# Kernel optimization log

Hardware: AMD Instinct MI355X
Metric: run time of the kernel (lower is better)

The kernel has to match this reference:

```python
import jax, jax.numpy as jnp
import numpy as np
import math

D_MODEL = 512
N_HEADS = 8
D_FF = 2048
TOP_FACTOR = 5
LN_EPS = 1e-5


def _layernorm(x, g, b):
    m = jnp.mean(x, axis=-1, keepdims=True)
    v = jnp.mean((x - m) ** 2, axis=-1, keepdims=True)
    return (x - m) / jnp.sqrt(v + LN_EPS) * g + b


def _prob_sparse_attn(q_in, k_in, v_in, wq, bq, wk, bk, wv, bv, wo, bo):
    # weights stored (in, out): y = x @ w + b  (equivalent to torch Linear)
    B, Lq, dm = q_in.shape
    Lk = k_in.shape[1]
    H, D = N_HEADS, dm // N_HEADS
    q = (q_in @ wq + bq).reshape(B, Lq, H, D).transpose(0, 2, 1, 3)  # (B,H,Lq,D)
    k = (k_in @ wk + bk).reshape(B, Lk, H, D).transpose(0, 2, 1, 3)
    v = (v_in @ wv + bv).reshape(B, Lk, H, D).transpose(0, 2, 1, 3)

    qn = q / jnp.linalg.norm(q, axis=-1, keepdims=True)
    kn = k / jnp.linalg.norm(k, axis=-1, keepdims=True)
    # full cosine-similarity matrix, reduced to a row mean (as in the original)
    scores_all = jnp.einsum('bhqd,bhkd->bhqk', qn, kn)
    mean_scores = scores_all.mean(axis=-1)  # (B,H,Lq)

    u = max(1, Lq // TOP_FACTOR)
    _, top_idx = jax.lax.top_k(mean_scores, u)  # (B,H,u)

    q_sel = jnp.take_along_axis(q, top_idx[..., None], axis=2)  # (B,H,u,D)
    scores = jnp.einsum('bhud,bhkd->bhuk', q_sel, k) / math.sqrt(D)
    attn = jax.nn.softmax(scores, axis=-1)
    ctx_sel = jnp.einsum('bhuk,bhkd->bhud', attn, v)  # (B,H,u,D)

    b_ix = jnp.arange(B)[:, None, None]
    h_ix = jnp.arange(H)[None, :, None]
    context = jnp.zeros((B, H, Lq, D), dtype=q.dtype).at[b_ix, h_ix, top_idx].set(ctx_sel)
    out = context.transpose(0, 2, 1, 3).reshape(B, Lq, dm)
    return out @ wo + bo


def _decoder_layer(x, enc_out, p):
    xn = _layernorm(x, p['ln1_g'], p['ln1_b'])
    x = x + _prob_sparse_attn(xn, xn, xn, p['sa_wq'], p['sa_bq'], p['sa_wk'], p['sa_bk'],
                              p['sa_wv'], p['sa_bv'], p['sa_wo'], p['sa_bo'])
    xn = _layernorm(x, p['ln2_g'], p['ln2_b'])
    x = x + _prob_sparse_attn(xn, enc_out, enc_out, p['ca_wq'], p['ca_bq'], p['ca_wk'], p['ca_bk'],
                              p['ca_wv'], p['ca_bv'], p['ca_wo'], p['ca_bo'])
    xn = _layernorm(x, p['ln3_g'], p['ln3_b'])
    h = jax.nn.relu(xn @ p['ff_w1'] + p['ff_b1'])
    return x + (h @ p['ff_w2'] + p['ff_b2'])


def setup_inputs() -> dict:
    key = jax.random.key(0)
    ks = iter(jax.random.split(key, 32))
    B, L = 2, 2048
    dm, dff = D_MODEL, D_FF
    s = 1.0 / math.sqrt(dm)
    inp = {
        'x': jax.random.normal(next(ks), (B, L, dm), jnp.float32),
        'enc_out': jax.random.normal(next(ks), (B, L, dm), jnp.float32),
    }
    for pre in ('sa', 'ca'):
        for nm in ('wq', 'wk', 'wv', 'wo'):
            inp[f'{pre}_{nm}'] = jax.random.normal(next(ks), (dm, dm), jnp.float32) * s
            inp[f'{pre}_{nm[1:] and "b" + nm[1:]}'] = jnp.zeros((dm,), jnp.float32)
    inp['ff_w1'] = jax.random.normal(next(ks), (dm, dff), jnp.float32) * s
    inp['ff_b1'] = jnp.zeros((dff,), jnp.float32)
    inp['ff_w2'] = jax.random.normal(next(ks), (dff, dm), jnp.float32) / math.sqrt(dff)
    inp['ff_b2'] = jnp.zeros((dm,), jnp.float32)
    for i in (1, 2, 3):
        inp[f'ln{i}_g'] = jnp.ones((dm,), jnp.float32)
        inp[f'ln{i}_b'] = jnp.zeros((dm,), jnp.float32)
    return inp


def reference(x, enc_out,
              sa_wq, sa_bq, sa_wk, sa_bk, sa_wv, sa_bv, sa_wo, sa_bo,
              ca_wq, ca_bq, ca_wk, ca_bk, ca_wv, ca_bv, ca_wo, ca_bo,
              ff_w1, ff_b1, ff_w2, ff_b2,
              ln1_g, ln1_b, ln2_g, ln2_b, ln3_g, ln3_b):
    p = dict(sa_wq=sa_wq, sa_bq=sa_bq, sa_wk=sa_wk, sa_bk=sa_bk, sa_wv=sa_wv, sa_bv=sa_bv,
             sa_wo=sa_wo, sa_bo=sa_bo, ca_wq=ca_wq, ca_bq=ca_bq, ca_wk=ca_wk, ca_bk=ca_bk,
             ca_wv=ca_wv, ca_bv=ca_bv, ca_wo=ca_wo, ca_bo=ca_bo,
             ff_w1=ff_w1, ff_b1=ff_b1, ff_w2=ff_w2, ff_b2=ff_b2,
             ln1_g=ln1_g, ln1_b=ln1_b, ln2_g=ln2_g, ln2_b=ln2_b, ln3_g=ln3_g, ln3_b=ln3_b)
    return _decoder_layer(x, enc_out, p)
```

## Files before the change

### kernel.cpp

```cpp
#include <hip/hip_runtime.h>

#define BB 2
#define LL 2048
#define DM 512
#define NH 8
#define DH 64
#define DFF 2048
#define UU 409
#define ROWS (BB*LL)
#define X_ELEMS 2097152
#define NCHUNK 16

typedef unsigned short u16;
typedef __attribute__((ext_vector_type(8))) short short8;
typedef __attribute__((ext_vector_type(4))) float floatx4;

#define G_TOTAL 38200000
__device__ float g_buf[G_TOTAL];
__device__ int   g_isbf16;

#define A_Q     10495488
#define A_K     12592640
#define A_V     14689792
#define A_MKN   25175552
#define A_MS    25176576
#define A_RANK  25209344
#define A_PARTK 25242112
#define A_LIST  25274880
#define A_PO    25281536
#define A_PML   33670144
#define A_CTXF  16786944
#define XN_H    16796672
#define XN_L    18893824
#define CTX_H   33573888
#define CTX_L   35671040
#define ENC_H   37768192
#define ENC_L   39865344
#define AH_H    41962496
#define WT_SAQKV 67864576
#define WT_SAO   69437440
#define WT_CAQ   69961728
#define WT_CAKV  70486016
#define WT_CAO   71534592
#define WT_W1    72058880
#define WT_W2    74156032

__constant__ int c_end[28] = {
    2097152, 4194304, 4456448, 4456960, 4719104, 4719616, 4981760, 4982272,
    5244416, 5244928, 5507072, 5507584, 5769728, 5770240, 6032384, 6032896,
    6295040, 6295552, 7344128, 7346176, 8394752, 8395264, 8395776, 8396288,
    8396800, 8397312, 8397824, 8398336
};
__constant__ int sm_idx[16] = {3,5,7,9,11,13,15,17,19,21,22,23,24,25,26,27};
__constant__ int sm_cum[16] = {64,128,192,256,320,384,448,512,768,832,896,960,1024,1088,1152,1216};
#define XG 262144
#define EG 262144
#define SG 1216

__device__ __forceinline__ float bf2f(u16 x) {
    union { unsigned int u; float f; } c; c.u = ((unsigned int)x) << 16; return c.f;
}
__device__ __forceinline__ u16 f2bf(float f) {
    union { float f; unsigned int u; } c; c.f = f;
    unsigned int u = c.u;
    return (u16)((u + 0x7FFFu + ((u >> 16) & 1u)) >> 16);
}

struct P28 { const void* p[28]; };
struct I3 { int v[3]; };

__constant__ int tj[10][6] = {
    {2,  WT_SAQKV, 0,    512,  786432, 8},
    {4,  WT_SAQKV, 512,  512,  786432, 8},
    {6,  WT_SAQKV, 1024, 512,  786432, 8},
    {8,  WT_SAO,   0,    512,  262144, 8},
    {10, WT_CAQ,   0,    512,  262144, 8},
    {12, WT_CAKV,  0,    512,  524288, 8},
    {14, WT_CAKV,  512,  512,  524288, 8},
    {16, WT_CAO,   0,    512,  262144, 8},
    {18, WT_W1,    0,    512, 1048576, 32},
    {20, WT_W2,    0,   2048, 1048576, 8},
};
__constant__ int tcum[10] = {64, 128, 192, 256, 320, 384, 448, 512, 768, 1024};
__global__ void prep_all(P28 ps) {
    const int f = (((const u16*)ps.p[22])[0] == 0x3F80u) ? 1 : 0;
    if (blockIdx.x == 0 && threadIdx.x == 0) g_isbf16 = f;
    u16* gb16 = (u16*)g_buf;
    if (blockIdx.x < 1024) {
        int bid = blockIdx.x;
        int j = 0;
        while (bid >= tcum[j]) j++;
        int t = bid - (j ? tcum[j - 1] : 0);
        int widx = tj[j][0], wt = tj[j][1], col0 = tj[j][2];
        int K = tj[j][3], lo = tj[j][4], txn = tj[j][5];
        int Nsrc = txn * 64;
        int n0 = (t % txn) * 64, k0 = (t / txn) * 64;
        __shared__ float tb[64][65];
        int c = threadIdx.x & 63, r0 = threadIdx.x >> 6;
        const void* W = ps.p[widx];
        u16* WTh = gb16 + wt;
        for (int i = 0; i < 16; i++) {
            int r = r0 + 4 * i;
            size_t src = (size_t)(k0 + r) * Nsrc + n0 + c;
            tb[r][c] = f ? bf2f(((const u16*)W)[src]) : ((const float*)W)[src];
        }
        __syncthreads();
        for (int i = 0; i < 16; i++) {
            int r = r0 + 4 * i;
            float v = tb[c][r];
            u16 hi = f2bf(v);
            size_t o = (size_t)(col0 + n0 + r) * K + k0 + c;
            WTh[o] = hi;
            WTh[lo + o] = f2bf(v - bf2f(hi));
        }
        return;
    }
    int stride = 2048 * blockDim.x;
    for (int g = (blockIdx.x - 1024) * blockDim.x + threadIdx.x; g < XG + EG + SG; g += stride) {
        if (g < XG) {
            int e = g * 8;
            if (f) {
                uint4 raw = ((const uint4*)ps.p[0])[g];
                const u16* rr = (const u16*)&raw;
                float v[8] __attribute__((aligned(16)));
#pragma unroll
                for (int i = 0; i < 8; i++) v[i] = bf2f(rr[i]);
                *(float4*)(g_buf + e) = ((const float4*)v)[0];
                *(float4*)(g_buf + e + 4) = ((const float4*)v)[1];
            } else {
                *(uint4*)(g_buf + e)     = ((const uint4*)ps.p[0])[g * 2];
                *(uint4*)(g_buf + e + 4) = ((const uint4*)ps.p[0])[g * 2 + 1];
            }
        } else if (g < XG + EG) {
            int gl = g - XG;
            int e = gl * 8;
            float v[8] __attribute__((aligned(16)));
            if (f) {
                uint4 raw = ((const uint4*)ps.p[1])[gl];
                const u16* rr = (const u16*)&raw;
#pragma unroll
                for (int i = 0; i < 8; i++) v[i] = bf2f(rr[i]);
            } else {
                *(float4*)(v)     = ((const float4*)ps.p[1])[gl * 2];
                *(float4*)(v + 4) = ((const float4*)ps.p[1])[gl * 2 + 1];
            }
            u16 hh[8] __attribute__((aligned(16)));
            u16 lo[8] __attribute__((aligned(16)));
#pragma unroll
            for (int i = 0; i < 8; i++) { u16 hi = f2bf(v[i]); hh[i] = hi; lo[i] = f2bf(v[i] - bf2f(hi)); }
            *(uint4*)(&gb16[ENC_H + e]) = *(const uint4*)hh;
            *(uint4*)(&gb16[ENC_L + e]) = *(const uint4*)lo;
        } else {
            int t = g - XG - EG;
            int si = 0;
            while (t >= sm_cum[si]) si++;
            int s = sm_idx[si];
            int gl = t - (si ? sm_cum[si - 1] : 0);
            int e = gl * 8;
            float* dst = g_buf + c_end[s - 1] + e;
            if (f) {
                uint4 raw = *(const uint4*)((const u16*)ps.p[s] + e);
                const u16* rr = (const u16*)&raw;
#pragma unroll
                for (int i = 0; i < 8; i++) dst[i] = bf2f(rr[i]);
            } else {
                *(uint4*)(dst)     = *(const uint4*)((const float*)ps.p[s] + e);
                *(uint4*)(dst + 4) = *(const uint4*)((const float*)ps.p[s] + e + 4);
            }
        }
    }
}

__global__ void lnorm_k(int x_off, int g_off, int b_off, int yh_u16, int yl_u16) {
    int row = blockIdx.x;
    int tid = threadIdx.x;
    const float* x = g_buf + x_off + (size_t)row * DM;
    float a = x[tid], c = x[tid + 256];
    float s1 = a + c, s2 = a * a + c * c;
    for (int o = 32; o > 0; o >>= 1) { s1 += __shfl_xor(s1, o); s2 += __shfl_xor(s2, o); }
    __shared__ float r1[4], r2[4];
    int wave = tid >> 6, lane = tid & 63;
    if (lane == 0) { r1[wave] = s1; r2[wave] = s2; }
    __syncthreads();
    s1 = r1[0] + r1[1] + r1[2] + r1[3];
    s2 = r2[0] + r2[1] + r2[2] + r2[3];
    float mean = s1 * (1.0f / DM);
    float var  = s2 * (1.0f / DM) - mean * mean;
    float rstd = rsqrtf(var + 1e-5f);
    const float* gg = g_buf + g_off;
    const float* bb = g_buf + b_off;
    u16* yh = ((u16*)g_buf) + yh_u16 + (size_t)row * DM;
    u16* yl = ((u16*)g_buf) + yl_u16 + (size_t)row * DM;
    float v1 = (a - mean) * rstd * gg[tid]       + bb[tid];
    float v2 = (c - mean) * rstd * gg[tid + 256] + bb[tid + 256];
    u16 h1 = f2bf(v1), h2 = f2bf(v2);
    yh[tid] = h1;       yl[tid] = f2bf(v1 - bf2f(h1));
    yh[tid + 256] = h2; yl[tid + 256] = f2bf(v2 - bf2f(h2));
}

template<int WM, bool SPLIT, bool SEC, bool RELU, bool RESID, bool FINAL, bool OUTH>
__global__ void mgemm_k(I3 a_offs, I3 splt, I3 alz, int wt_u16_off, I3 boffs, int resid_off,
                        int out_off, void* __restrict__ dext, int M, int N, int K) {
    constexpr int BT_M = WM * 32;
    constexpr int A4 = BT_M * 4;
    __shared__ u16 Ash[BT_M * 40];
    __shared__ u16 Asl[SPLIT ? BT_M * 40 : 8];
    __shared__ u16 Bsh[128 * 40];
    __shared__ u16 Bsl[SPLIT ? 128 * 40 : 8];
    int sec_blk = SEC ? ((blockIdx.x * 128) >> 9) : 0;
    const u16* Ah = ((const u16*)g_buf) + a_offs.v[sec_blk];
    const u16* Al = Ah + (size_t)M * K;
    const u16* WTh = ((const u16*)g_buf) + wt_u16_off;
    const u16* WTl = WTh + (size_t)N * K;
    const int isbf = g_isbf16;
    const bool use_al = SPLIT && splt.v[sec_blk] && !(alz.v[sec_blk] && isbf);
    const bool use_bl = SPLIT && splt.v[sec_blk] && !isbf;
    int tid = threadIdx.x;
    int lane = tid & 63, wid = tid >> 6;
    int wm = wid >> 1, wn = wid & 1;
    int quad = lane >> 4, l15 = lane & 15;
    int m0 = blockIdx.y * BT_M, n0 = blockIdx.x * 128;
    floatx4 acc[WM][4];
#pragma unroll
    for (int i = 0; i < WM; i++)
#pragma unroll
        for (int j = 0; j < 4; j++) acc[i][j] = (floatx4){0.f, 0.f, 0.f, 0.f};
    for (int k0 = 0; k0 < K; k0 += 32) {
#pragma unroll
        for (int i = 0; i < (A4 + 255) / 256; i++) {
            int idx8 = tid + 256 * i;
            if (A4 % 256 == 0 || idx8 < A4) {
                int r = idx8 >> 2, c8 = (idx8 & 3) * 8;
                *(uint4*)(&Ash[r * 40 + c8]) = *(const uint4*)(Ah + (size_t)(m0 + r) * K + k0 + c8);
                if (SPLIT && use_al)
                    *(uint4*)(&Asl[r * 40 + c8]) = *(const uint4*)(Al + (size_t)(m0 + r) * K + k0 + c8);
            }
        }
#pragma unroll
        for (int i = 0; i < 2; i++) {
            int idx8 = tid + 256 * i;
            int r = idx8 >> 2, c8 = (idx8 & 3) * 8;
            *(uint4*)(&Bsh[r * 40 + c8]) = *(const uint4*)(WTh + (size_t)(n0 + r) * K + k0 + c8);
            if (SPLIT && use_bl)
                *(uint4*)(&Bsl[r * 40 + c8]) = *(const uint4*)(WTl + (size_t)(n0 + r) * K + k0 + c8);
        }
        __syncthreads();
        short8 ah[WM], bh[4], al[WM], bl[4];
#pragma unroll
        for (int i = 0; i < WM; i++) {
            int ro = (wm * WM * 16 + i * 16 + l15) * 40 + quad * 8;
            ah[i] = *(const short8*)(&Ash[ro]);
            if (SPLIT && use_al) al[i] = *(const short8*)(&Asl[ro]);
        }
#pragma unroll
        for (int j = 0; j < 4; j++) {
            int ro = (wn * 64 + j * 16 + l15) * 40 + quad * 8;
            bh[j] = *(const short8*)(&Bsh[ro]);
            if (SPLIT && use_bl) bl[j] = *(const short8*)(&Bsl[ro]);
        }
#pragma unroll
        for (int i = 0; i < WM; i++)
#pragma unroll
            for (int j = 0; j < 4; j++) {
                acc[i][j] = __builtin_amdgcn_mfma_f32_16x16x32_bf16(ah[i], bh[j], acc[i][j], 0, 0, 0);
                if constexpr (SPLIT) {
                    if (use_bl)
                        acc[i][j] = __builtin_amdgcn_mfma_f32_16x16x32_bf16(ah[i], bl[j], acc[i][j], 0, 0, 0);
                    if (use_al)
                        acc[i][j] = __builtin_amdgcn_mfma_f32_16x16x32_bf16(al[i], bh[j], acc[i][j], 0, 0, 0);
                }
            }
        __syncthreads();
    }
#pragma unroll
    for (int i = 0; i < WM; i++)
#pragma unroll
        for (int j = 0; j < 4; j++)
#pragma unroll
            for (int r = 0; r < 4; r++) {
                int row = m0 + wm * WM * 16 + i * 16 + quad * 4 + r;
                int col = n0 + wn * 64 + j * 16 + l15;
                int sec = SEC ? (col >> 9) : 0;
                int ci  = SEC ? (col & 511) : col;
                float v = acc[i][j][r] + g_buf[boffs.v[sec] + ci];
                if (RELU) v = fmaxf(v, 0.f);
                if (RESID) v += g_buf[resid_off + (size_t)row * N + col];
                if (FINAL) {
                    if (g_isbf16) ((u16*)dext)[(size_t)row * N + col] = f2bf(v);
                    else          ((float*)dext)[(size_t)row * N + col] = v;
                } else if (OUTH) {
                    ((u16*)g_buf)[out_off + (size_t)row * N + col] = f2bf(v);
                } else if (SEC) {
                    g_buf[out_off + ((size_t)sec * ROWS + row) * 512 + ci] = v;
                } else {
                    g_buf[out_off + (size_t)row * N + col] = v;
                }
            }
}

__global__ void meankn_p1(int k_off, int part_off) {
    int bh = blockIdx.x >> 5, chunk = blockIdx.x & 31;
    int b = bh >> 3, h = bh & 7;
    int wave = threadIdx.x >> 6, lane = threadIdx.x & 63;
    const float* base = g_buf + k_off + (size_t)b * LL * DM + (size_t)h * DH + lane;
    float acc = 0.f;
    for (int t = 0; t < 16; t++) {
        int j = chunk * 64 + wave * 16 + t;
        float kv = base[(size_t)j * DM];
        float s = kv * kv;
        for (int o = 32; o > 0; o >>= 1) s += __shfl_xor(s, o);
        acc += kv / sqrtf(fmaxf(s, 1e-30f));
    }
    __shared__ float red[4][64];
    red[wave][lane] = acc;
    __syncthreads();
    if (threadIdx.x < 64)
        g_buf[part_off + (size_t)blockIdx.x * 64 + threadIdx.x] =
            red[0][threadIdx.x] + red[1][threadIdx.x] + red[2][threadIdx.x] + red[3][threadIdx.x];
}

__global__ void mscore_k(int q_off, int part_off, int ms_off) {
    int bh = blockIdx.y, b = bh >> 3, h = bh & 7;
    int tid = threadIdx.x;
    __shared__ float mk[64];
    if (tid < 64) {
        float s = 0.f;
        for (int c = 0; c < 32; c++) s += g_buf[part_off + (size_t)(bh * 32 + c) * 64 + tid];
        mk[tid] = s * (1.0f / LL);
    }
    __syncthreads();
    int w = tid >> 6, lane = tid & 63;
    float m = mk[lane];
#pragma unroll
    for (int it = 0; it < 8; it++) {
        int row = blockIdx.x * 32 + it * 4 + w;
        float qv = g_buf[q_off + ((size_t)b * LL + row) * DM + h * DH + lane];
        float s = qv * qv, d = qv * m;
        for (int o = 32; o > 0; o >>= 1) { s += __shfl_xor(s, o); d += __shfl_xor(d, o); }
        if (lane == 0) g_buf[ms_off + bh * LL + row] = d / sqrtf(fmaxf(s, 1e-30f));
    }
}

__global__ void topsel_k(int ms_off, int list_off, int rank_off, int u) {
    __shared__ float s[LL];
    int bh = blockIdx.y, chunk = blockIdx.x;
    for (int i = threadIdx.x; i < LL; i += 256) s[i] = g_buf[ms_off + bh * LL + i];
    __syncthreads();
    int il = threadIdx.x >> 2;
    int i = chunk * 64 + il;
    int jq = threadIdx.x & 3;
    float si = s[i];
    int cnt = 0;
    for (int t = 0; t < 512; t++) {
        int j = jq * 512 + t;
        float sj = s[j];
        cnt += (sj > si) || (sj == si && j < i);
    }
    cnt += __shfl_xor(cnt, 1);
    cnt += __shfl_xor(cnt, 2);
    if (jq == 0) {
        int* list = (int*)(g_buf + list_off);
        int* rank = (int*)(g_buf + rank_off);
        if (cnt < u) { list[bh * 416 + cnt] = i; rank[bh * LL + i] = cnt; }
        else rank[bh * LL + i] = -1;
    }
}

template<bool S3>
__global__ __launch_bounds__(256) void attn_flash(int q_off, int k_off, int v_off,
        int list_off, int po_off, int pml_off, int u) {
    int bh = blockIdx.y, b = bh >> 3, h = bh & 7;
    int chunk = blockIdx.z;
    int tid = threadIdx.x, lane = tid & 63, w = tid >> 6;
    int quad = lane >> 4, l15 = lane & 15;
    const int* list = (const int*)(g_buf + list_off);

    short8 qh[2][2], ql[2][2];
#pragma unroll
    for (int g = 0; g < 2; g++) {
        int slot_q = blockIdx.x * 128 + w * 32 + g * 16 + l15;
        int qidx = list[bh * 416 + (slot_q < u ? slot_q : u - 1)];
        const float* qp = g_buf + q_off + ((size_t)b * LL + qidx) * DM + h * DH;
#pragma unroll
        for (int d2 = 0; d2 < 2; d2++) {
            float v[8] __attribute__((aligned(16)));
            *(float4*)(v)     = *(const float4*)(qp + d2 * 32 + quad * 8);
            *(float4*)(v + 4) = *(const float4*)(qp + d2 * 32 + quad * 8 + 4);
            u16 hh[8] __attribute__((aligned(16)));
            u16 lo[8] __attribute__((aligned(16)));
#pragma unroll
            for (int j = 0; j < 8; j++) {
                float s = v[j] * 0.125f;
                u16 hi = f2bf(s); hh[j] = hi; lo[j] = f2bf(s - bf2f(hi));
            }
            qh[g][d2] = *(const short8*)hh; ql[g][d2] = *(const short8*)lo;
        }
    }

    __shared__ u16 Ksh[64 * 68];
    __shared__ u16 Ksl[S3 ? 64 * 68 : 8];
    __shared__ u16 Vth[64 * 68];
    __shared__ u16 Vtl[S3 ? 64 * 68 : 8];
    __shared__ float smbuf[4352];

    float m_run[2][4], l_run[2][4];
    floatx4 acc_o[2][4];
#pragma unroll
    for (int g = 0; g < 2; g++)
#pragma unroll
        for (int r = 0; r < 4; r++) {
            m_run[g][r] = -3.0e38f; l_run[g][r] = 0.f;
            acc_o[g][r] = (floatx4){0.f, 0.f, 0.f, 0.f};
        }

    for (int kt = 0; kt < 2; kt++) {
        int row0 = chunk * 128 + kt * 64;
        __syncthreads();
        {
            int tok = tid >> 2, c = (tid & 3) * 16;
            const float* kp = g_buf + k_off + ((size_t)(b * LL + row0 + tok)) * DM + h * DH + c;
            float v[16] __attribute__((aligned(16)));
#pragma unroll
            for (int i = 0; i < 4; i++) *(float4*)(v + 4 * i) = *(const float4*)(kp + 4 * i);
            u16 hh[16] __attribute__((aligned(16)));
#pragma unroll
            for (int i = 0; i < 16; i++) hh[i] = f2bf(v[i]);
            *(uint4*)(&Ksh[tok * 68 + c])     = ((const uint4*)hh)[0];
            *(uint4*)(&Ksh[tok * 68 + c + 8]) = ((const uint4*)hh)[1];
            if constexpr (S3) {
                u16 lo[16] __attribute__((aligned(16)));
#pragma unroll
                for (int i = 0; i < 16; i++) lo[i] = f2bf(v[i] - bf2f(hh[i]));
                *(uint4*)(&Ksl[tok * 68 + c])     = ((const uint4*)lo)[0];
                *(uint4*)(&Ksl[tok * 68 + c + 8]) = ((const uint4*)lo)[1];
            }
            const float* vp = g_buf + v_off + ((size_t)(b * LL + row0 + tok)) * DM + h * DH + c;
#pragma unroll
            for (int i = 0; i < 4; i++)
                *(float4*)(&smbuf[tok * 68 + c + 4 * i]) = *(const float4*)(vp + 4 * i);
        }
        __syncthreads();
        {
            int d = tid >> 2, ck = (tid & 3) * 16;
            u16 hh[16] __attribute__((aligned(16)));
            float xv[16];
#pragma unroll
            for (int i = 0; i < 16; i++) { xv[i] = smbuf[(ck + i) * 68 + d]; hh[i] = f2bf(xv[i]); }
            *(uint4*)(&Vth[d * 68 + ck])     = ((const uint4*)hh)[0];
            *(uint4*)(&Vth[d * 68 + ck + 8]) = ((const uint4*)hh)[1];
            if constexpr (S3) {
                u16 lo[16] __attribute__((aligned(16)));
#pragma unroll
                for (int i = 0; i < 16; i++) lo[i] = f2bf(xv[i] - bf2f(hh[i]));
                *(uint4*)(&Vtl[d * 68 + ck])     = ((const uint4*)lo)[0];
                *(uint4*)(&Vtl[d * 68 + ck + 8]) = ((const uint4*)lo)[1];
            }
        }
        __syncthreads();
        float* ps = smbuf + w * 1088;
#pragma unroll
        for (int g = 0; g < 2; g++) {
            floatx4 sacc[4];
#pragma unroll
            for (int t = 0; t < 4; t++) {
                sacc[t] = (floatx4){0.f, 0.f, 0.f, 0.f};
#pragma unroll
                for (int d2 = 0; d2 < 2; d2++) {
                    int ro = (t * 16 + l15) * 68 + d2 * 32 + quad * 8;
                    short8 kh = *(const short8*)(&Ksh[ro]);
                    sacc[t] = __builtin_amdgcn_mfma_f32_16x16x32_bf16(qh[g][d2], kh, sacc[t], 0, 0, 0);
                    sacc[t] = __builtin_amdgcn_mfma_f32_16x16x32_bf16(ql[g][d2], kh, sacc[t], 0, 0, 0);
                    if constexpr (S3) {
                        short8 kl = *(const short8*)(&Ksl[ro]);
                        sacc[t] = __builtin_amdgcn_mfma_f32_16x16x32_bf16(qh[g][d2], kl, sacc[t], 0, 0, 0);
                    }
                }
            }
            float alpha[4];
#pragma unroll
            for (int r = 0; r < 4; r++) {
                float mx = fmaxf(fmaxf(sacc[0][r], sacc[1][r]), fmaxf(sacc[2][r], sacc[3][r]));
                for (int o = 1; o < 16; o <<= 1) mx = fmaxf(mx, __shfl_xor(mx, o));
                float mn = fmaxf(m_run[g][r], mx);
                alpha[r] = __expf(m_run[g][r] - mn);
                m_run[g][r] = mn;
                float ls = 0.f;
#pragma unroll
                for (int t = 0; t < 4; t++) {
                    float p = __expf(sacc[t][r] - mn);
                    sacc[t][r] = p;
                    ls += p;
                }
                for (int o = 1; o < 16; o <<= 1) ls += __shfl_xor(ls, o);
                l_run[g][r] = l_run[g][r] * alpha[r] + ls;
            }
#pragma unroll
            for (int t = 0; t < 4; t++)
#pragma unroll
                for (int r = 0; r < 4; r++)
                    ps[(quad * 4 + r) * 68 + t * 16 + l15] = sacc[t][r];
#pragma unroll
            for (int j = 0; j < 4; j++)
#pragma unroll
                for (int r = 0; r < 4; r++) acc_o[g][j][r] *= alpha[r];
#pragma unroll
            for (int s2 = 0; s2 < 2; s2++) {
                float pv[8] __attribute__((aligned(16)));
                *(float4*)(pv)     = *(const float4*)(&ps[l15 * 68 + s2 * 32 + quad * 8]);
                *(float4*)(pv + 4) = *(const float4*)(&ps[l15 * 68 + s2 * 32 + quad * 8 + 4]);
                u16 ph[8] __attribute__((aligned(16)));
                u16 pl[8] __attribute__((aligned(16)));
#pragma unroll
                for (int j = 0; j < 8; j++) { u16 hi = f2bf(pv[j]); ph[j] = hi; pl[j] = f2bf(pv[j] - bf2f(hi)); }
                short8 phv = *(const short8*)ph, plv = *(const short8*)pl;
#pragma unroll
                for (int j = 0; j < 4; j++) {
                    int ro = (j * 16 + l15) * 68 + s2 * 32 + quad * 8;
                    short8 vh = *(const short8*)(&Vth[ro]);
                    acc_o[g][j] = __builtin_amdgcn_mfma_f32_16x16x32_bf16(phv, vh, acc_o[g][j], 0, 0, 0);
                    acc_o[g][j] = __builtin_amdgcn_mfma_f32_16x16x32_bf16(plv, vh, acc_o[g][j], 0, 0, 0);
                    if constexpr (S3) {
                        short8 vl = *(const short8*)(&Vtl[ro]);
                        acc_o[g][j] = __builtin_amdgcn_mfma_f32_16x16x32_bf16(phv, vl, acc_o[g][j], 0, 0, 0);
                    }
                }
            }
        }
    }
#pragma unroll
    for (int g = 0; g < 2; g++)
#pragma unroll
        for (int r = 0; r < 4; r++) {
            int slot = blockIdx.x * 128 + w * 32 + g * 16 + quad * 4 + r;
            if (slot >= u) continue;
            size_t rec = ((size_t)(bh * 16 + chunk)) * 512 + slot;
            float* po = g_buf + po_off + rec * 64;
#pragma unroll
            for (int j = 0; j < 4; j++) po[j * 16 + l15] = acc_o[g][j][r];
            if (l15 == 0) {
                float* pml = g_buf + pml_off + rec * 2;
                pml[0] = m_run[g][r]; pml[1] = l_run[g][r];
            }
        }
}

__global__ void attn_combine(int po_off, int pml_off, int rank_off, int u) {
    int bh = blockIdx.y;
    int b = bh >> 3, h = bh & 7;
    int tid = threadIdx.x;
    int qi = tid >> 4;
    int kb = tid & 15;
    int ds = kb * 4;
    int row = blockIdx.x * 16 + qi;
    int rank = ((const int*)(g_buf + rank_off))[bh * LL + row];
    size_t idx = ((size_t)b * LL + row) * DM + h * DH + ds;
    if (rank < 0) {
        ushort4 z = {0, 0, 0, 0};
        *(ushort4*)(((u16*)g_buf) + CTX_H + idx) = z;
        *(ushort4*)(((u16*)g_buf) + CTX_L + idx) = z;
        return;
    }
    float m = -3.0e38f;
#pragma unroll
    for (int c = 0; c < NCHUNK; c++)
        m = fmaxf(m, g_buf[pml_off + (((size_t)(bh * 16 + c)) * 512 + rank) * 2]);
    float l = 0.f, O0 = 0.f, O1 = 0.f, O2 = 0.f, O3 = 0.f;
#pragma unroll
    for (int c = 0; c < NCHUNK; c++) {
        size_t rec = ((size_t)(bh * 16 + c)) * 512 + rank;
        const float* pml = g_buf + pml_off + rec * 2;
        float a = __expf(pml[0] - m);
        l += a * pml[1];
        float4 o = *(const float4*)(g_buf + po_off + rec * 64 + ds);
        O0 += a * o.x; O1 += a * o.y; O2 += a * o.z; O3 += a * o.w;
    }
    float inv = 1.0f / l;
    float o0 = O0 * inv, o1 = O1 * inv, o2 = O2 * inv, o3 = O3 * inv;
    ushort4 hv, lv;
    hv.x = f2bf(o0); lv.x = f2bf(o0 - bf2f(hv.x));
    hv.y = f2bf(o1); lv.y = f2bf(o1 - bf2f(hv.y));
    hv.z = f2bf(o2); lv.z = f2bf(o2 - bf2f(hv.z));
    hv.w = f2bf(o3); lv.w = f2bf(o3 - bf2f(hv.w));
    *(ushort4*)(((u16*)g_buf) + CTX_H + idx) = hv;
    *(ushort4*)(((u16*)g_buf) + CTX_L + idx) = lv;
}

extern "C" void kernel_launch(void* const* d_in, const int* in_sizes, int n_in,
                              void* d_out, int out_size, void* d_ws, size_t ws_size,
                              hipStream_t stream) {
    static const int SZ[28] = {
        2097152, 2097152,
        262144, 512, 262144, 512, 262144, 512, 262144, 512,
        262144, 512, 262144, 512, 262144, 512, 262144, 512,
        1048576, 2048, 1048576, 512,
        512, 512, 512, 512, 512, 512
    };
    int OFF[28];
    int cur = 0;
    for (int i = 0; i < 28; i++) { OFF[i] = cur; cur += SZ[i]; }

    P28 ps;
    for (int i = 0; i < 28; i++) ps.p[i] = d_in[i];
    prep_all<<<3072, 256, 0, stream>>>(ps);

    auto select_attend = [&](bool sa) {
        meankn_p1<<<16 * 32, 256, 0, stream>>>(A_K, A_PARTK);
        mscore_k<<<dim3(64, 16), 256, 0, stream>>>(A_Q, A_PARTK, A_MS);
        topsel_k<<<dim3(32, 16), 256, 0, stream>>>(A_MS, A_LIST, A_RANK, UU);
        if (sa)
            attn_flash<true><<<dim3(4, 16, NCHUNK), 256, 0, stream>>>(A_Q, A_K, A_V, A_LIST, A_PO, A_PML, UU);
        else
            attn_flash<false><<<dim3(4, 16, NCHUNK), 256, 0, stream>>>(A_Q, A_K, A_V, A_LIST, A_PO, A_PML, UU);
        attn_combine<<<dim3(128, 16), 256, 0, stream>>>(A_PO, A_PML, A_RANK, UU);
    };

    lnorm_k<<<ROWS, 256, 0, stream>>>(OFF[0], OFF[22], OFF[23], XN_H, XN_L);
    mgemm_k<2, true, true, false, false, false, false><<<dim3(12, 64), 256, 0, stream>>>(
        I3{{XN_H, XN_H, XN_H}}, I3{{1, 1, 1}}, I3{{0, 0, 0}},
        WT_SAQKV, I3{{OFF[3], OFF[5], OFF[7]}}, 0, A_Q, nullptr, ROWS, 1536, 512);
    select_attend(true);
    mgemm_k<1, true, false, false, true, false, false><<<dim3(4, 128), 256, 0, stream>>>(
        I3{{CTX_H, 0, 0}}, I3{{1, 0, 0}}, I3{{0, 0, 0}},
        WT_SAO, I3{{OFF[9], 0, 0}}, OFF[0], OFF[0], nullptr, ROWS, 512, 512);

    lnorm_k<<<ROWS, 256, 0, stream>>>(OFF[0], OFF[24], OFF[25], XN_H, XN_L);
    mgemm_k<1, true, false, false, false, false, false><<<dim3(4, 128), 256, 0, stream>>>(
        I3{{XN_H, 0, 0}}, I3{{1, 0, 0}}, I3{{0, 0, 0}},
        WT_CAQ, I3{{OFF[11], 0, 0}}, 0, A_Q, nullptr, ROWS, 512, 512);
    mgemm_k<2, true, true, false, false, false, false><<<dim3(8, 64), 256, 0, stream>>>(
        I3{{ENC_H, ENC_H, ENC_H}}, I3{{1, 0, 0}}, I3{{1, 0, 0}},
        WT_CAKV, I3{{OFF[13], OFF[15], 0}}, 0, A_K, nullptr, ROWS, 1024, 512);
    select_attend(false);
    mgemm_k<1, false, false, false, true, false, false><<<dim3(4, 128), 256, 0, stream>>>(
        I3{{CTX_H, 0, 0}}, I3{{0, 0, 0}}, I3{{0, 0, 0}},
        WT_CAO, I3{{OFF[17], 0, 0}}, OFF[0], OFF[0], nullptr, ROWS, 512, 512);

    lnorm_k<<<ROWS, 256, 0, stream>>>(OFF[0], OFF[26], OFF[27], XN_H, XN_L);
    mgemm_k<4, false, false, true, false, false, true><<<dim3(16, 32), 256, 0, stream>>>(
        I3{{XN_H, 0, 0}}, I3{{0, 0, 0}}, I3{{0, 0, 0}},
        WT_W1, I3{{OFF[19], 0, 0}}, 0, AH_H, nullptr, ROWS, 2048, 512);
    mgemm_k<1, false, false, false, true, true, false><<<dim3(4, 128), 256, 0, stream>>>(
        I3{{AH_H, 0, 0}}, I3{{0, 0, 0}}, I3{{0, 0, 0}},
        WT_W2, I3{{OFF[21], 0, 0}}, OFF[0], 0, d_out, ROWS, 512, 2048);
}
```

Measured before the change: 567.3 us.

## Precompute bf16 K/V-transpose once and prefetch tiles in flash attention

Adds a kvprep kernel that converts K and V to bf16 hi/lo split form once per head, with V stored transposed, in global scratch. The flash-attention kernel then loads ready-made bf16 tiles through a register prefetch (issue/commit) that overlaps the next tile's global loads with the current tile's compute. It no longer converts and transposes K/V in every block. NCHUNK is halved so each block handles 256 keys instead of 128, reducing the partial results the combine kernel has to merge, at the cost of less parallelism in the attention grid and an extra launch.

```diff
diff --git a/kernel.cpp b/kernel.cpp
--- a/kernel.cpp
+++ b/kernel.cpp
@@ -9,7 +9,7 @@
 #define UU 409
 #define ROWS (BB*LL)
 #define X_ELEMS 2097152
-#define NCHUNK 16
+#define NCHUNK 8
 
 typedef unsigned short u16;
 typedef __attribute__((ext_vector_type(8))) short short8;
@@ -28,7 +28,7 @@
 #define A_PARTK 25242112
 #define A_LIST  25274880
 #define A_PO    25281536
-#define A_PML   33670144
+#define A_PML   29475840
 #define A_CTXF  16786944
 #define XN_H    16796672
 #define XN_L    18893824
@@ -37,6 +37,10 @@
 #define ENC_H   37768192
 #define ENC_L   39865344
 #define AH_H    41962496
+#define KH16    59213824
+#define KL16    61310976
+#define VTH16   63408128
+#define VTL16   65505280
 #define WT_SAQKV 67864576
 #define WT_SAO   69437440
 #define WT_CAQ   69961728
@@ -366,9 +370,51 @@
     }
 }
 
+template<bool LO>
+__global__ void kvprep_k(int k_off, int v_off) {
+    int bh = blockIdx.y, b = bh >> 3, h = bh & 7;
+    int tok0 = blockIdx.x * 64;
+    int tid = threadIdx.x;
+    __shared__ float vt[64][68];
+    u16* gb16 = (u16*)g_buf;
+    int tok = tid >> 2, dq = (tid & 3) * 16;
+    const float* kp = g_buf + k_off + ((size_t)(b * LL + tok0 + tok)) * DM + h * DH + dq;
+    const float* vp = g_buf + v_off + ((size_t)(b * LL + tok0 + tok)) * DM + h * DH + dq;
+    float kv[16] __attribute__((aligned(16)));
+#pragma unroll
+    for (int i = 0; i < 4; i++) *(float4*)(kv + 4 * i) = *(const float4*)(kp + 4 * i);
+    u16 hh[16] __attribute__((aligned(16)));
+    u16 lo[16] __attribute__((aligned(16)));
+#pragma unroll
+    for (int i = 0; i < 16; i++) { hh[i] = f2bf(kv[i]); if (LO) lo[i] = f2bf(kv[i] - bf2f(hh[i])); }
+    size_t ko = ((size_t)(bh * LL + tok0 + tok)) * DH + dq;
+    *(uint4*)(gb16 + KH16 + ko)     = ((const uint4*)hh)[0];
+    *(uint4*)(gb16 + KH16 + ko + 8) = ((const uint4*)hh)[1];
+    if (LO) {
+        *(uint4*)(gb16 + KL16 + ko)     = ((const uint4*)lo)[0];
+        *(uint4*)(gb16 + KL16 + ko + 8) = ((const uint4*)lo)[1];
+    }
+#pragma unroll
+    for (int i = 0; i < 4; i++) *(float4*)(&vt[tok][dq + 4 * i]) = *(const float4*)(vp + 4 * i);
+    __syncthreads();
+    int d = tid >> 2, tq = (tid & 3) * 16;
+    float vv[16];
+#pragma unroll
+    for (int i = 0; i < 16; i++) vv[i] = vt[tq + i][d];
+#pragma unroll
+    for (int i = 0; i < 16; i++) { hh[i] = f2bf(vv[i]); if (LO) lo[i] = f2bf(vv[i] - bf2f(hh[i])); }
+    size_t vo = ((size_t)(bh * DH + d)) * LL + tok0 + tq;
+    *(uint4*)(gb16 + VTH16 + vo)     = ((const uint4*)hh)[0];
+    *(uint4*)(gb16 + VTH16 + vo + 8) = ((const uint4*)hh)[1];
+    if (LO) {
+        *(uint4*)(gb16 + VTL16 + vo)     = ((const uint4*)lo)[0];
+        *(uint4*)(gb16 + VTL16 + vo + 8) = ((const uint4*)lo)[1];
+    }
+}
+
 template<bool S3>
-__global__ __launch_bounds__(256) void attn_flash(int q_off, int k_off, int v_off,
-        int list_off, int po_off, int pml_off, int u) {
+__global__ __launch_bounds__(256) void attn_flash(int q_off, int kh_off, int kl_off,
+        int vth_off, int vtl_off, int list_off, int po_off, int pml_off, int u) {
     int bh = blockIdx.y, b = bh >> 3, h = bh & 7;
     int chunk = blockIdx.z;
     int tid = threadIdx.x, lane = tid & 63, w = tid >> 6;
@@ -403,6 +449,40 @@
     __shared__ u16 Vtl[S3 ? 64 * 68 : 8];
     __shared__ float smbuf[4352];
 
+    const u16* gb16 = (const u16*)g_buf;
+    const u16* KHp = gb16 + kh_off + (size_t)bh * LL * DH;
+    const u16* KLp = gb16 + kl_off + (size_t)bh * LL * DH;
+    const u16* VHp = gb16 + vth_off + (size_t)bh * DH * LL;
+    const u16* VLp = gb16 + vtl_off + (size_t)bh * DH * LL;
+    int r8 = tid >> 3;
+    int gg = (tid & 7) * 8;
+
+    uint4 pre[S3 ? 8 : 4];
+    auto issue = [&](int row0) {
+#pragma unroll
+        for (int it = 0; it < 2; ++it) {
+            int r = r8 + 32 * it;
+            pre[it * (S3 ? 4 : 2) + 0] = *(const uint4*)(KHp + (size_t)(row0 + r) * DH + gg);
+            pre[it * (S3 ? 4 : 2) + 1] = *(const uint4*)(VHp + (size_t)r * LL + row0 + gg);
+            if constexpr (S3) {
+                pre[it * 4 + 2] = *(const uint4*)(KLp + (size_t)(row0 + r) * DH + gg);
+                pre[it * 4 + 3] = *(const uint4*)(VLp + (size_t)r * LL + row0 + gg);
+            }
+        }
+    };
+    auto commit = [&]() {
+#pragma unroll
+        for (int it = 0; it < 2; ++it) {
+            int r = r8 + 32 * it;
+            *(uint4*)(&Ksh[r * 68 + gg]) = pre[it * (S3 ? 4 : 2) + 0];
+            *(uint4*)(&Vth[r * 68 + gg]) = pre[it * (S3 ? 4 : 2) + 1];
+            if constexpr (S3) {
+                *(uint4*)(&Ksl[r * 68 + gg]) = pre[it * 4 + 2];
+                *(uint4*)(&Vtl[r * 68 + gg]) = pre[it * 4 + 3];
+            }
+        }
+    };
+
     float m_run[2][4], l_run[2][4];
     floatx4 acc_o[2][4];
 #pragma unroll
@@ -413,49 +493,11 @@
             acc_o[g][r] = (floatx4){0.f, 0.f, 0.f, 0.f};
         }
 
-    for (int kt = 0; kt < 2; kt++) {
-        int row0 = chunk * 128 + kt * 64;
+    issue(chunk * 256);
+    for (int kt = 0; kt < 4; ++kt) {
         __syncthreads();
-        {
-            int tok = tid >> 2, c = (tid & 3) * 16;
-            const float* kp = g_buf + k_off + ((size_t)(b * LL + row0 + tok)) * DM + h * DH + c;
-            float v[16] __attribute__((aligned(16)));
-#pragma unroll
-            for (int i = 0; i < 4; i++) *(float4*)(v + 4 * i) = *(const float4*)(kp + 4 * i);
-            u16 hh[16] __attribute__((aligned(16)));
-#pragma unroll
-            for (int i = 0; i < 16; i++) hh[i] = f2bf(v[i]);
-            *(uint4*)(&Ksh[tok * 68 + c])     = ((const uint4*)hh)[0];
-            *(uint4*)(&Ksh[tok * 68 + c + 8]) = ((const uint4*)hh)[1];
-            if constexpr (S3) {
-                u16 lo[16] __attribute__((aligned(16)));
-#pragma unroll
-                for (int i = 0; i < 16; i++) lo[i] = f2bf(v[i] - bf2f(hh[i]));
-                *(uint4*)(&Ksl[tok * 68 + c])     = ((const uint4*)lo)[0];
-                *(uint4*)(&Ksl[tok * 68 + c + 8]) = ((const uint4*)lo)[1];
-            }
-            const float* vp = g_buf + v_off + ((size_t)(b * LL + row0 + tok)) * DM + h * DH + c;
-#pragma unroll
-            for (int i = 0; i < 4; i++)
-                *(float4*)(&smbuf[tok * 68 + c + 4 * i]) = *(const float4*)(vp + 4 * i);
-        }
-        __syncthreads();
-        {
-            int d = tid >> 2, ck = (tid & 3) * 16;
-            u16 hh[16] __attribute__((aligned(16)));
-            float xv[16];
-#pragma unroll
-            for (int i = 0; i < 16; i++) { xv[i] = smbuf[(ck + i) * 68 + d]; hh[i] = f2bf(xv[i]); }
-            *(uint4*)(&Vth[d * 68 + ck])     = ((const uint4*)hh)[0];
-            *(uint4*)(&Vth[d * 68 + ck + 8]) = ((const uint4*)hh)[1];
-            if constexpr (S3) {
-                u16 lo[16] __attribute__((aligned(16)));
-#pragma unroll
-                for (int i = 0; i < 16; i++) lo[i] = f2bf(xv[i] - bf2f(hh[i]));
-                *(uint4*)(&Vtl[d * 68 + ck])     = ((const uint4*)lo)[0];
-                *(uint4*)(&Vtl[d * 68 + ck + 8]) = ((const uint4*)lo)[1];
-            }
-        }
+        commit();
+        if (kt < 3) issue(chunk * 256 + (kt + 1) * 64);
         __syncthreads();
         float* ps = smbuf + w * 1088;
 #pragma unroll
@@ -533,7 +575,7 @@
         for (int r = 0; r < 4; r++) {
             int slot = blockIdx.x * 128 + w * 32 + g * 16 + quad * 4 + r;
             if (slot >= u) continue;
-            size_t rec = ((size_t)(bh * 16 + chunk)) * 512 + slot;
+            size_t rec = ((size_t)(bh * NCHUNK + chunk)) * 512 + slot;
             float* po = g_buf + po_off + rec * 64;
 #pragma unroll
             for (int j = 0; j < 4; j++) po[j * 16 + l15] = acc_o[g][j][r];
@@ -563,11 +605,11 @@
     float m = -3.0e38f;
 #pragma unroll
     for (int c = 0; c < NCHUNK; c++)
-        m = fmaxf(m, g_buf[pml_off + (((size_t)(bh * 16 + c)) * 512 + rank) * 2]);
+        m = fmaxf(m, g_buf[pml_off + (((size_t)(bh * NCHUNK + c)) * 512 + rank) * 2]);
     float l = 0.f, O0 = 0.f, O1 = 0.f, O2 = 0.f, O3 = 0.f;
 #pragma unroll
     for (int c = 0; c < NCHUNK; c++) {
-        size_t rec = ((size_t)(bh * 16 + c)) * 512 + rank;
+        size_t rec = ((size_t)(bh * NCHUNK + c)) * 512 + rank;
         const float* pml = g_buf + pml_off + rec * 2;
         float a = __expf(pml[0] - m);
         l += a * pml[1];
@@ -604,13 +646,17 @@
     prep_all<<<3072, 256, 0, stream>>>(ps);
 
     auto select_attend = [&](bool sa) {
+        if (sa) kvprep_k<true><<<dim3(32, 16), 256, 0, stream>>>(A_K, A_V);
+        else    kvprep_k<false><<<dim3(32, 16), 256, 0, stream>>>(A_K, A_V);
         meankn_p1<<<16 * 32, 256, 0, stream>>>(A_K, A_PARTK);
         mscore_k<<<dim3(64, 16), 256, 0, stream>>>(A_Q, A_PARTK, A_MS);
         topsel_k<<<dim3(32, 16), 256, 0, stream>>>(A_MS, A_LIST, A_RANK, UU);
         if (sa)
-            attn_flash<true><<<dim3(4, 16, NCHUNK), 256, 0, stream>>>(A_Q, A_K, A_V, A_LIST, A_PO, A_PML, UU);
+            attn_flash<true><<<dim3(4, 16, NCHUNK), 256, 0, stream>>>(
+                A_Q, KH16, KL16, VTH16, VTL16, A_LIST, A_PO, A_PML, UU);
         else
-            attn_flash<false><<<dim3(4, 16, NCHUNK), 256, 0, stream>>>(A_Q, A_K, A_V, A_LIST, A_PO, A_PML, UU);
+            attn_flash<false><<<dim3(4, 16, NCHUNK), 256, 0, stream>>>(
+                A_Q, KH16, KL16, VTH16, VTL16, A_LIST, A_PO, A_PML, UU);
         attn_combine<<<dim3(128, 16), 256, 0, stream>>>(A_PO, A_PML, A_RANK, UU);
     };
 
```

Result: no change. 576.8 us (+1.7%).
